# Optimization experiments

Measured on AMD Instinct MI355X. Metric: run time of the kernel, lower is better.

The kernel has to match this reference:

```python
import jax, jax.numpy as jnp
import numpy as np

N_NODES = 100000
N_EDGES = 1600000
D_IN = 128
D_OUT = 128


def setup_inputs() -> dict:
    key = jax.random.key(0)
    kx, ke, kw = jax.random.split(key, 3)
    x = jax.random.normal(kx, (N_NODES, D_IN), dtype=jnp.float32)
    edge_index = jax.random.randint(ke, (2, N_EDGES), 0, N_NODES, dtype=jnp.int32)
    W = jax.random.normal(kw, (D_IN, D_OUT), dtype=jnp.float32) / np.sqrt(D_IN)
    b = jnp.zeros((D_OUT,), dtype=jnp.float32)
    return {"x": x, "edge_index": edge_index, "W": W, "b": b}


def reference(x, edge_index, W, b):
    # PyG GCNConv: x' = D^{-1/2} (A + I) D^{-1/2} (x @ W) + b, then ReLU.
    n = x.shape[0]
    xw = x @ W  # linear transform first (as in GCNConv)
    # add self-loops
    loops = jnp.arange(n, dtype=edge_index.dtype)
    row = jnp.concatenate([edge_index[0], loops])  # source nodes
    col = jnp.concatenate([edge_index[1], loops])  # destination nodes
    # symmetric degree normalization (degree counted on destination, PyG-style)
    deg = jax.ops.segment_sum(jnp.ones_like(col, dtype=xw.dtype), col, num_segments=n)
    dinv = jnp.where(deg > 0, jax.lax.rsqrt(deg), 0.0)
    norm = dinv[row] * dinv[col]  # [E+N]
    # gather -> scale -> scatter-add
    msg = xw[row] * norm[:, None]  # [E+N, D_OUT]
    agg = jax.ops.segment_sum(msg, col, num_segments=n)  # [N, D_OUT]
    return jax.nn.relu(agg + b)
```

## Files before the change

### kernel.cpp

```cpp
#include <hip/hip_runtime.h>

#define DCH 128
#define T_PART 4096
#define B_MAX 512
#define CAPC 6144

typedef short bf16x8 __attribute__((ext_vector_type(8)));
typedef float f32x4 __attribute__((ext_vector_type(4)));

__device__ inline unsigned short f2bf(float f) {
    unsigned int u = __float_as_uint(f);
    unsigned int r = (u + 0x7fffu + ((u >> 16) & 1u)) >> 16;
    return (unsigned short)r;
}

__device__ inline void gload_lds16(const void* g, void* l) {
    __builtin_amdgcn_global_load_lds(
        (const __attribute__((address_space(1))) void*)g,
        (__attribute__((address_space(3))) void*)l, 16, 0, 0);
}

__global__ __launch_bounds__(512) void k_pg(const int* __restrict__ row,
                                            const int* __restrict__ col,
                                            unsigned int* __restrict__ coarse,
                                            int* __restrict__ gcount,
                                            const float* __restrict__ W,
                                            unsigned short* __restrict__ Wf,
                                            int E, int B, int nPart) {
    int tid = threadIdx.x;
    int wv = tid >> 6, lane = tid & 63;

    if (blockIdx.x >= nPart) {
        int frag = (blockIdx.x - nPart) * 8 + wv;
        if (frag < 32) {
            int nt = frag >> 2, ks = frag & 3;
            int nn = nt * 16 + (lane & 15);
            int k0 = ks * 32 + ((lane >> 4) * 8);
            unsigned short tmp[8];
#pragma unroll
            for (int j = 0; j < 8; ++j) tmp[j] = f2bf(W[(size_t)(k0 + j) * DCH + nn]);
            *(uint4*)&Wf[((size_t)frag * 64 + lane) * 8] = *(const uint4*)tmp;
        }
        return;
    }

    __shared__ unsigned int spack[T_PART];
    __shared__ unsigned short sbuck[T_PART];
    __shared__ int hist[B_MAX];
    __shared__ int basex[B_MAX];
    __shared__ int curx[B_MAX];
    __shared__ int wsum[8];
    int* gb = hist;

    int base_e = blockIdx.x * T_PART;
    int tileCnt = min(T_PART, E - base_e);

    hist[tid] = 0;
    __syncthreads();

    int er[8], ec[8];
#pragma unroll
    for (int i = 0; i < 8; ++i) {
        int e = base_e + tid + i * 512;
        if (e < E) {
            er[i] = row[e];
            ec[i] = col[e];
            atomicAdd(&hist[ec[i] >> 8], 1);
        } else {
            er[i] = -1;
            ec[i] = 0;
        }
    }
    __syncthreads();

    int v = hist[tid];
    int x2 = v;
#pragma unroll
    for (int o = 1; o < 64; o <<= 1) {
        int t = __shfl_up(x2, o, 64);
        if (lane >= o) x2 += t;
    }
    if (lane == 63) wsum[wv] = x2;
    __syncthreads();
    int add = 0;
    for (int w = 0; w < wv; ++w) add += wsum[w];
    int excl = x2 - v + add;
    basex[tid] = excl;
    curx[tid] = excl;
    gb[tid] = (tid < B && v > 0) ? atomicAdd(&gcount[tid], v) : 0;
    __syncthreads();

#pragma unroll
    for (int i = 0; i < 8; ++i) {
        if (er[i] >= 0) {
            int bb = ec[i] >> 8;
            int slot = atomicAdd(&curx[bb], 1);
            spack[slot] = ((unsigned int)er[i] << 8) | (unsigned int)(ec[i] & 255);
            sbuck[slot] = (unsigned short)bb;
        }
    }
    __syncthreads();

    for (int s = tid; s < tileCnt; s += 512) {
        int bb = sbuck[s];
        int dst = gb[bb] + (s - basex[bb]);
        if (dst < CAPC) coarse[(size_t)bb * CAPC + dst] = spack[s];
    }
}

__global__ __launch_bounds__(512) void k_cg(const unsigned int* __restrict__ coarse,
                                            const int* __restrict__ gcount,
                                            int* __restrict__ srow,
                                            int* __restrict__ off,
                                            float* __restrict__ dinvf,
                                            const float* __restrict__ x,
                                            const unsigned short* __restrict__ Wf,
                                            unsigned short* __restrict__ y,
                                            int n, int B) {
    __shared__ uint4 smem4[2048];
    char* smem = (char*)smem4;

    int tid = threadIdx.x;
    int wv = tid >> 6, lane = tid & 63;

    if (blockIdx.x < B) {
        unsigned int* ent = (unsigned int*)smem;
        int* h   = (int*)(smem + 24576);
        int* cur = (int*)(smem + 25600);
        int* red1 = (int*)(smem + 26624);
        int* red2 = (int*)(smem + 26656);
        int* bbase_p = (int*)(smem + 26672);

        int b = blockIdx.x;

        int part = 0;
        for (int i = tid; i < b; i += 512) part += gcount[i];
#pragma unroll
        for (int o = 1; o < 64; o <<= 1) part += __shfl_xor(part, o, 64);
        if (lane == 0) red1[wv] = part;
        if (tid < 256) h[tid] = 0;
        __syncthreads();
        if (tid == 0) {
            int s = 0;
            for (int w = 0; w < 8; ++w) s += red1[w];
            bbase_p[0] = s;
        }
        int cntb = min(gcount[b], CAPC);
        for (int s = tid; s < cntb; s += 512) ent[s] = coarse[(size_t)b * CAPC + s];
        __syncthreads();

        for (int s = tid; s < cntb; s += 512) atomicAdd(&h[ent[s] & 255], 1);
        __syncthreads();

        int x2 = 0, v = 0;
        if (tid < 256) {
            v = h[tid];
            x2 = v;
#pragma unroll
            for (int o = 1; o < 64; o <<= 1) {
                int t = __shfl_up(x2, o, 64);
                if (lane >= o) x2 += t;
            }
            if (lane == 63) red2[wv] = x2;
        }
        __syncthreads();
        int bbase = bbase_p[0];
        if (tid < 256) {
            int add = 0;
            for (int w = 0; w < wv; ++w) add += red2[w];
            int excl = x2 - v + add;
            cur[tid] = excl;
            int node = (b << 8) + tid;
            if (node < n) {
                off[node] = bbase + excl;
                dinvf[node] = rsqrtf((float)(v + 1));
            }
        }
        __syncthreads();

        for (int s = tid; s < cntb; s += 512) {
            unsigned int p = ent[s];
            int d = p & 255;
            int slot = atomicAdd(&cur[d], 1);
            srow[bbase + slot] = (int)(p >> 8);
        }
    } else {
        int blockRow = (blockIdx.x - B) * 64;

#pragma unroll
        for (int t = 0; t < 4; ++t) {
            int off2 = t * 8192 + wv * 1024 + lane * 16;
            int r = off2 >> 9;
            int gr = blockRow + r;
            if (gr >= n) gr = n - 1;
            int colb = (off2 & 511) ^ ((r & 7) << 4);
            const char* src = (const char*)x + (size_t)gr * 512 + colb;
            char* dst = smem + t * 8192 + wv * 1024;
            gload_lds16(src, dst);
        }
        __syncthreads();

        f32x4 acc[4];
        f32x4 zero = {0.f, 0.f, 0.f, 0.f};
#pragma unroll
        for (int t = 0; t < 4; ++t) acc[t] = zero;

        const bf16x8* wfv = (const bf16x8*)Wf;
        int rowL = (wv >> 1) * 16 + (lane & 15);
        int ntBase = (wv & 1) * 4;
        int q = lane >> 4;
        int swz = (rowL & 7) << 4;
#pragma unroll
        for (int ks = 0; ks < 4; ++ks) {
            int colb = ks * 128 + q * 32;
            float4 lo = *(const float4*)&smem[(rowL * 512 + colb) ^ swz];
            float4 hi = *(const float4*)&smem[(rowL * 512 + colb + 16) ^ swz];
            bf16x8 a;
            a[0] = (short)f2bf(lo.x); a[1] = (short)f2bf(lo.y);
            a[2] = (short)f2bf(lo.z); a[3] = (short)f2bf(lo.w);
            a[4] = (short)f2bf(hi.x); a[5] = (short)f2bf(hi.y);
            a[6] = (short)f2bf(hi.z); a[7] = (short)f2bf(hi.w);
#pragma unroll
            for (int nt2 = 0; nt2 < 4; ++nt2) {
                int nt = ntBase + nt2;
                bf16x8 bfr = wfv[(nt * 4 + ks) * 64 + lane];
                acc[nt2] = __builtin_amdgcn_mfma_f32_16x16x32_bf16(a, bfr, acc[nt2], 0, 0, 0);
            }
        }

        int rowBase = blockRow + (wv >> 1) * 16;
        int orow_base = rowBase + q * 4;
#pragma unroll
        for (int r = 0; r < 4; ++r) {
            int orow = orow_base + r;
            if (orow < n) {
#pragma unroll
                for (int nt2 = 0; nt2 < 4; ++nt2) {
                    int nt = ntBase + nt2;
                    y[(size_t)orow * DCH + nt * 16 + (lane & 15)] = f2bf(acc[nt2][r]);
                }
            }
        }
    }
}

__global__ __launch_bounds__(256) void k_agg(const uint4* __restrict__ y4,
                                             const int* __restrict__ srow,
                                             const int* __restrict__ off,
                                             const float* __restrict__ dinv,
                                             const float* __restrict__ b,
                                             float* __restrict__ out, int n, int E) {
    int i = blockIdx.x * 4 + (threadIdx.x >> 6);
    if (i >= n) return;
    int lane = threadIdx.x & 63;
    int q = lane >> 4;
    int l16 = lane & 15;
    int s = off[i];
    int e = (i + 1 < n) ? off[i + 1] : E;
    float di = dinv[i];

    float acc[8];
#pragma unroll
    for (int k = 0; k < 8; ++k) acc[k] = 0.f;

    if (q == 0) {
        uint4 v = y4[(size_t)i * 16 + l16];
        unsigned int p[4] = {v.x, v.y, v.z, v.w};
#pragma unroll
        for (int t = 0; t < 4; ++t) {
            acc[2 * t]     = fmaf(di, __uint_as_float(p[t] << 16), acc[2 * t]);
            acc[2 * t + 1] = fmaf(di, __uint_as_float(p[t] & 0xffff0000u), acc[2 * t + 1]);
        }
    }

    int j = s;
    for (; j + 16 <= e; j += 16) {
        int s0 = srow[j + q];
        int s1 = srow[j + 4 + q];
        int s2 = srow[j + 8 + q];
        int s3 = srow[j + 12 + q];
        float d0 = dinv[s0], d1 = dinv[s1], d2 = dinv[s2], d3 = dinv[s3];
        uint4 v0 = y4[(size_t)s0 * 16 + l16];
        uint4 v1 = y4[(size_t)s1 * 16 + l16];
        uint4 v2 = y4[(size_t)s2 * 16 + l16];
        uint4 v3 = y4[(size_t)s3 * 16 + l16];
        unsigned int p0[4] = {v0.x, v0.y, v0.z, v0.w};
        unsigned int p1[4] = {v1.x, v1.y, v1.z, v1.w};
        unsigned int p2[4] = {v2.x, v2.y, v2.z, v2.w};
        unsigned int p3[4] = {v3.x, v3.y, v3.z, v3.w};
#pragma unroll
        for (int t = 0; t < 4; ++t) {
            acc[2 * t]     = fmaf(d0, __uint_as_float(p0[t] << 16), acc[2 * t]);
            acc[2 * t + 1] = fmaf(d0, __uint_as_float(p0[t] & 0xffff0000u), acc[2 * t + 1]);
            acc[2 * t]     = fmaf(d1, __uint_as_float(p1[t] << 16), acc[2 * t]);
            acc[2 * t + 1] = fmaf(d1, __uint_as_float(p1[t] & 0xffff0000u), acc[2 * t + 1]);
            acc[2 * t]     = fmaf(d2, __uint_as_float(p2[t] << 16), acc[2 * t]);
            acc[2 * t + 1] = fmaf(d2, __uint_as_float(p2[t] & 0xffff0000u), acc[2 * t + 1]);
            acc[2 * t]     = fmaf(d3, __uint_as_float(p3[t] << 16), acc[2 * t]);
            acc[2 * t + 1] = fmaf(d3, __uint_as_float(p3[t] & 0xffff0000u), acc[2 * t + 1]);
        }
    }
    for (; j + 8 <= e; j += 8) {
        int s0 = srow[j + q];
        int s1 = srow[j + 4 + q];
        float d0 = dinv[s0], d1 = dinv[s1];
        uint4 v0 = y4[(size_t)s0 * 16 + l16];
        uint4 v1 = y4[(size_t)s1 * 16 + l16];
        unsigned int p0[4] = {v0.x, v0.y, v0.z, v0.w};
        unsigned int p1[4] = {v1.x, v1.y, v1.z, v1.w};
#pragma unroll
        for (int t = 0; t < 4; ++t) {
            acc[2 * t]     = fmaf(d0, __uint_as_float(p0[t] << 16), acc[2 * t]);
            acc[2 * t + 1] = fmaf(d0, __uint_as_float(p0[t] & 0xffff0000u), acc[2 * t + 1]);
            acc[2 * t]     = fmaf(d1, __uint_as_float(p1[t] << 16), acc[2 * t]);
            acc[2 * t + 1] = fmaf(d1, __uint_as_float(p1[t] & 0xffff0000u), acc[2 * t + 1]);
        }
    }
    for (; j + 4 <= e; j += 4) {
        int s0 = srow[j + q];
        float d0 = dinv[s0];
        uint4 v0 = y4[(size_t)s0 * 16 + l16];
        unsigned int p0[4] = {v0.x, v0.y, v0.z, v0.w};
#pragma unroll
        for (int t = 0; t < 4; ++t) {
            acc[2 * t]     = fmaf(d0, __uint_as_float(p0[t] << 16), acc[2 * t]);
            acc[2 * t + 1] = fmaf(d0, __uint_as_float(p0[t] & 0xffff0000u), acc[2 * t + 1]);
        }
    }
    if (j + q < e) {
        int s0 = srow[j + q];
        float d0 = dinv[s0];
        uint4 v0 = y4[(size_t)s0 * 16 + l16];
        unsigned int p0[4] = {v0.x, v0.y, v0.z, v0.w};
#pragma unroll
        for (int t = 0; t < 4; ++t) {
            acc[2 * t]     = fmaf(d0, __uint_as_float(p0[t] << 16), acc[2 * t]);
            acc[2 * t + 1] = fmaf(d0, __uint_as_float(p0[t] & 0xffff0000u), acc[2 * t + 1]);
        }
    }

#pragma unroll
    for (int k = 0; k < 8; ++k) {
        acc[k] += __shfl_xor(acc[k], 16, 64);
        acc[k] += __shfl_xor(acc[k], 32, 64);
    }

    if (q == 0) {
        float sc = di;
        int c0 = l16 * 8;
        float4 b0 = *(const float4*)&b[c0];
        float4 b1 = *(const float4*)&b[c0 + 4];
        f32x4 o0, o1;
        o0[0] = fmaxf(fmaf(sc, acc[0], b0.x), 0.f);
        o0[1] = fmaxf(fmaf(sc, acc[1], b0.y), 0.f);
        o0[2] = fmaxf(fmaf(sc, acc[2], b0.z), 0.f);
        o0[3] = fmaxf(fmaf(sc, acc[3], b0.w), 0.f);
        o1[0] = fmaxf(fmaf(sc, acc[4], b1.x), 0.f);
        o1[1] = fmaxf(fmaf(sc, acc[5], b1.y), 0.f);
        o1[2] = fmaxf(fmaf(sc, acc[6], b1.z), 0.f);
        o1[3] = fmaxf(fmaf(sc, acc[7], b1.w), 0.f);
        f32x4* orow = (f32x4*)&out[(size_t)i * DCH + c0];
        __builtin_nontemporal_store(o0, &orow[0]);
        __builtin_nontemporal_store(o1, &orow[1]);
    }
}

extern "C" void kernel_launch(void* const* d_in, const int* in_sizes, int n_in,
                              void* d_out, int out_size, void* d_ws, size_t ws_size,
                              hipStream_t stream) {
    const float* x = (const float*)d_in[0];
    const int* ei  = (const int*)d_in[1];
    const float* W = (const float*)d_in[2];
    const float* b = (const float*)d_in[3];
    float* out = (float*)d_out;

    int n = in_sizes[0] / DCH;
    int E = in_sizes[1] / 2;
    const int* row = ei;
    const int* col = ei + E;

    int B = (n + 255) / 256;

    char* ws = (char*)d_ws;
    size_t o = 0;
    auto alloc = [&](size_t bytes) -> void* {
        o = (o + 255) & ~(size_t)255;
        void* p = ws + o;
        o += bytes;
        return p;
    };
    float* dinvf = (float*)alloc((size_t)n * 4);
    int* off     = (int*)alloc((size_t)(n + 1) * 4);
    int* gcount  = (int*)alloc((size_t)B * 4);
    int* srow    = (int*)alloc((size_t)E * 4);
    unsigned int* coarse = (unsigned int*)alloc((size_t)B * CAPC * 4);
    unsigned short* Wf = (unsigned short*)alloc((size_t)DCH * DCH * 2);
    unsigned short* y  = (unsigned short*)alloc((size_t)n * DCH * 2);

    int nt = (E + T_PART - 1) / T_PART;
    int gemmBlocks = (n + 63) / 64;

    hipMemsetAsync(gcount, 0, (size_t)B * 4, stream);
    k_pg<<<nt + 4, 512, 0, stream>>>(row, col, coarse, gcount, W, Wf, E, B, nt);
    k_cg<<<B + gemmBlocks, 512, 0, stream>>>(coarse, gcount, srow, off, dinvf,
                                             x, Wf, y, n, B);
    k_agg<<<(n + 3) / 4, 256, 0, stream>>>((const uint4*)y, srow, off, dinvf,
                                           b, out, n, E);
}
```

Before: 201.4 us.

## Replace two-level bucket CSR build with global atomic histogram and scatter

Replaces the coarse bucket partition (local sort into fixed-capacity buckets, then per-bucket fine sort) with a direct CSR build: a per-node global atomic histogram, a per-block offset scan kernel, and a scatter kernel that claims slots with global atomics on per-node cursors. This removes the coarse intermediate buffer, its capacity limit, and the LDS sorting passes. In exchange it adds an extra kernel launch and two global atomics per edge, and the edge order within each node becomes nondeterministic.

```diff
diff --git a/kernel.cpp b/kernel.cpp
--- a/kernel.cpp
+++ b/kernel.cpp
@@ -1,9 +1,8 @@
 #include <hip/hip_runtime.h>
 
 #define DCH 128
-#define T_PART 4096
+#define T_EDGE 4096
 #define B_MAX 512
-#define CAPC 6144
 
 typedef short bf16x8 __attribute__((ext_vector_type(8)));
 typedef float f32x4 __attribute__((ext_vector_type(4)));
@@ -20,18 +19,17 @@
         (__attribute__((address_space(3))) void*)l, 16, 0, 0);
 }
 
-__global__ __launch_bounds__(512) void k_pg(const int* __restrict__ row,
-                                            const int* __restrict__ col,
-                                            unsigned int* __restrict__ coarse,
-                                            int* __restrict__ gcount,
-                                            const float* __restrict__ W,
-                                            unsigned short* __restrict__ Wf,
-                                            int E, int B, int nPart) {
+__global__ __launch_bounds__(512) void k_hist(const int* __restrict__ col,
+                                              int* __restrict__ cnt,
+                                              int* __restrict__ gcount,
+                                              const float* __restrict__ W,
+                                              unsigned short* __restrict__ Wf,
+                                              int E, int B, int nEB) {
     int tid = threadIdx.x;
     int wv = tid >> 6, lane = tid & 63;
 
-    if (blockIdx.x >= nPart) {
-        int frag = (blockIdx.x - nPart) * 8 + wv;
+    if (blockIdx.x >= nEB) {
+        int frag = (blockIdx.x - nEB) * 8 + wv;
         if (frag < 32) {
             int nt = frag >> 2, ks = frag & 3;
             int nn = nt * 16 + (lane & 15);
@@ -44,148 +42,109 @@
         return;
     }
 
-    __shared__ unsigned int spack[T_PART];
-    __shared__ unsigned short sbuck[T_PART];
-    __shared__ int hist[B_MAX];
-    __shared__ int basex[B_MAX];
-    __shared__ int curx[B_MAX];
-    __shared__ int wsum[8];
-    int* gb = hist;
-
-    int base_e = blockIdx.x * T_PART;
-    int tileCnt = min(T_PART, E - base_e);
-
-    hist[tid] = 0;
-    __syncthreads();
-
-    int er[8], ec[8];
+    __shared__ int bh[B_MAX];
+    bh[tid] = 0;
+    __syncthreads();
+
+    int base_e = blockIdx.x * T_EDGE;
 #pragma unroll
     for (int i = 0; i < 8; ++i) {
         int e = base_e + tid + i * 512;
         if (e < E) {
-            er[i] = row[e];
-            ec[i] = col[e];
-            atomicAdd(&hist[ec[i] >> 8], 1);
-        } else {
-            er[i] = -1;
-            ec[i] = 0;
-        }
-    }
-    __syncthreads();
-
-    int v = hist[tid];
-    int x2 = v;
-#pragma unroll
-    for (int o = 1; o < 64; o <<= 1) {
-        int t = __shfl_up(x2, o, 64);
-        if (lane >= o) x2 += t;
-    }
-    if (lane == 63) wsum[wv] = x2;
-    __syncthreads();
-    int add = 0;
-    for (int w = 0; w < wv; ++w) add += wsum[w];
-    int excl = x2 - v + add;
-    basex[tid] = excl;
-    curx[tid] = excl;
-    gb[tid] = (tid < B && v > 0) ? atomicAdd(&gcount[tid], v) : 0;
-    __syncthreads();
-
-#pragma unroll
-    for (int i = 0; i < 8; ++i) {
-        if (er[i] >= 0) {
-            int bb = ec[i] >> 8;
-            int slot = atomicAdd(&curx[bb], 1);
-            spack[slot] = ((unsigned int)er[i] << 8) | (unsigned int)(ec[i] & 255);
-            sbuck[slot] = (unsigned short)bb;
-        }
-    }
-    __syncthreads();
-
-    for (int s = tid; s < tileCnt; s += 512) {
-        int bb = sbuck[s];
-        int dst = gb[bb] + (s - basex[bb]);
-        if (dst < CAPC) coarse[(size_t)bb * CAPC + dst] = spack[s];
-    }
-}
-
-__global__ __launch_bounds__(512) void k_cg(const unsigned int* __restrict__ coarse,
-                                            const int* __restrict__ gcount,
-                                            int* __restrict__ srow,
-                                            int* __restrict__ off,
-                                            float* __restrict__ dinvf,
-                                            const float* __restrict__ x,
-                                            const unsigned short* __restrict__ Wf,
-                                            unsigned short* __restrict__ y,
-                                            int n, int B) {
+            int c = col[e];
+            atomicAdd(&cnt[c], 1);
+            atomicAdd(&bh[c >> 8], 1);
+        }
+    }
+    __syncthreads();
+    if (tid < B && bh[tid] > 0) atomicAdd(&gcount[tid], bh[tid]);
+}
+
+__global__ __launch_bounds__(512) void k_off(const int* __restrict__ cnt,
+                                             const int* __restrict__ gcount,
+                                             int* __restrict__ off,
+                                             int* __restrict__ cur,
+                                             float* __restrict__ dinvf,
+                                             int n, int B) {
+    __shared__ int red1[8], red2[4];
+    __shared__ int bbase_s;
+
+    int b = blockIdx.x;
+    int tid = threadIdx.x;
+    int wv = tid >> 6, lane = tid & 63;
+
+    int part = 0;
+    for (int i = tid; i < b; i += 512) part += gcount[i];
+#pragma unroll
+    for (int o = 1; o < 64; o <<= 1) part += __shfl_xor(part, o, 64);
+    if (lane == 0) red1[wv] = part;
+    __syncthreads();
+    if (tid == 0) {
+        int s = 0;
+        for (int w = 0; w < 8; ++w) s += red1[w];
+        bbase_s = s;
+    }
+    __syncthreads();
+
+    int x2 = 0, v = 0;
+    if (tid < 256) {
+        int node = (b << 8) + tid;
+        v = (node < n) ? cnt[node] : 0;
+        x2 = v;
+#pragma unroll
+        for (int o = 1; o < 64; o <<= 1) {
+            int t = __shfl_up(x2, o, 64);
+            if (lane >= o) x2 += t;
+        }
+        if (lane == 63) red2[wv] = x2;
+    }
+    __syncthreads();
+    if (tid < 256) {
+        int add = 0;
+        for (int w = 0; w < wv; ++w) add += red2[w];
+        int excl = x2 - v + add;
+        int node = (b << 8) + tid;
+        if (node < n) {
+            int o2 = bbase_s + excl;
+            off[node] = o2;
+            cur[node] = o2;
+            dinvf[node] = rsqrtf((float)(v + 1));
+        }
+    }
+}
+
+__global__ __launch_bounds__(512) void k_scat(const int* __restrict__ row,
+                                              const int* __restrict__ col,
+                                              int* __restrict__ cur,
+                                              int* __restrict__ srow,
+                                              const float* __restrict__ x,
+                                              const unsigned short* __restrict__ Wf,
+                                              unsigned short* __restrict__ y,
+                                              int E, int n, int nEB) {
     __shared__ uint4 smem4[2048];
     char* smem = (char*)smem4;
 
     int tid = threadIdx.x;
     int wv = tid >> 6, lane = tid & 63;
 
-    if (blockIdx.x < B) {
-        unsigned int* ent = (unsigned int*)smem;
-        int* h   = (int*)(smem + 24576);
-        int* cur = (int*)(smem + 25600);
-        int* red1 = (int*)(smem + 26624);
-        int* red2 = (int*)(smem + 26656);
-        int* bbase_p = (int*)(smem + 26672);
-
-        int b = blockIdx.x;
-
-        int part = 0;
-        for (int i = tid; i < b; i += 512) part += gcount[i];
-#pragma unroll
-        for (int o = 1; o < 64; o <<= 1) part += __shfl_xor(part, o, 64);
-        if (lane == 0) red1[wv] = part;
-        if (tid < 256) h[tid] = 0;
-        __syncthreads();
-        if (tid == 0) {
-            int s = 0;
-            for (int w = 0; w < 8; ++w) s += red1[w];
-            bbase_p[0] = s;
-        }
-        int cntb = min(gcount[b], CAPC);
-        for (int s = tid; s < cntb; s += 512) ent[s] = coarse[(size_t)b * CAPC + s];
-        __syncthreads();
-
-        for (int s = tid; s < cntb; s += 512) atomicAdd(&h[ent[s] & 255], 1);
-        __syncthreads();
-
-        int x2 = 0, v = 0;
-        if (tid < 256) {
-            v = h[tid];
-            x2 = v;
-#pragma unroll
-            for (int o = 1; o < 64; o <<= 1) {
-                int t = __shfl_up(x2, o, 64);
-                if (lane >= o) x2 += t;
-            }
-            if (lane == 63) red2[wv] = x2;
-        }
-        __syncthreads();
-        int bbase = bbase_p[0];
-        if (tid < 256) {
-            int add = 0;
-            for (int w = 0; w < wv; ++w) add += red2[w];
-            int excl = x2 - v + add;
-            cur[tid] = excl;
-            int node = (b << 8) + tid;
-            if (node < n) {
-                off[node] = bbase + excl;
-                dinvf[node] = rsqrtf((float)(v + 1));
-            }
-        }
-        __syncthreads();
-
-        for (int s = tid; s < cntb; s += 512) {
-            unsigned int p = ent[s];
-            int d = p & 255;
-            int slot = atomicAdd(&cur[d], 1);
-            srow[bbase + slot] = (int)(p >> 8);
-        }
+    if (blockIdx.x < nEB) {
+        int base_e = blockIdx.x * T_EDGE;
+        int er[8], ec[8];
+#pragma unroll
+        for (int i = 0; i < 8; ++i) {
+            int e = base_e + tid + i * 512;
+            er[i] = (e < E) ? row[e] : -1;
+            ec[i] = (e < E) ? col[e] : 0;
+        }
+        int sl[8];
+#pragma unroll
+        for (int i = 0; i < 8; ++i)
+            sl[i] = (er[i] >= 0) ? atomicAdd(&cur[ec[i]], 1) : 0;
+#pragma unroll
+        for (int i = 0; i < 8; ++i)
+            if (er[i] >= 0) srow[sl[i]] = er[i];
     } else {
-        int blockRow = (blockIdx.x - B) * 64;
+        int blockRow = (blockIdx.x - nEB) * 64;
 
 #pragma unroll
         for (int t = 0; t < 4; ++t) {
@@ -389,21 +348,23 @@
         o += bytes;
         return p;
     };
+    int* cnt     = (int*)alloc((size_t)(n + B) * 4);
+    int* gcount  = cnt + n;
     float* dinvf = (float*)alloc((size_t)n * 4);
     int* off     = (int*)alloc((size_t)(n + 1) * 4);
-    int* gcount  = (int*)alloc((size_t)B * 4);
+    int* cur     = (int*)alloc((size_t)n * 4);
     int* srow    = (int*)alloc((size_t)E * 4);
-    unsigned int* coarse = (unsigned int*)alloc((size_t)B * CAPC * 4);
     unsigned short* Wf = (unsigned short*)alloc((size_t)DCH * DCH * 2);
     unsigned short* y  = (unsigned short*)alloc((size_t)n * DCH * 2);
 
-    int nt = (E + T_PART - 1) / T_PART;
+    int nEB = (E + T_EDGE - 1) / T_EDGE;
     int gemmBlocks = (n + 63) / 64;
 
-    hipMemsetAsync(gcount, 0, (size_t)B * 4, stream);
-    k_pg<<<nt + 4, 512, 0, stream>>>(row, col, coarse, gcount, W, Wf, E, B, nt);
-    k_cg<<<B + gemmBlocks, 512, 0, stream>>>(coarse, gcount, srow, off, dinvf,
-                                             x, Wf, y, n, B);
+    hipMemsetAsync(cnt, 0, (size_t)(n + B) * 4, stream);
+    k_hist<<<nEB + 4, 512, 0, stream>>>(col, cnt, gcount, W, Wf, E, B, nEB);
+    k_off<<<B, 512, 0, stream>>>(cnt, gcount, off, cur, dinvf, n, B);
+    k_scat<<<nEB + gemmBlocks, 512, 0, stream>>>(row, col, cur, srow,
+                                                 x, Wf, y, E, n, nEB);
     k_agg<<<(n + 3) / 4, 256, 0, stream>>>((const uint4*)y, srow, off, dinvf,
                                            b, out, n, E);
 }
```

Result: slower. 331.9 us (+64.8%).

## Merge partition, GEMM and bucket-sort stages into one persistent cooperative kernel

Applied to the files above, without the earlier changes.

Replaces the separate partition and bucket-sort/GEMM launches with a single cooperative persistent kernel. Its blocks loop over edge-partition tiles and GEMM tiles, then meet at a grid-wide sync before the per-bucket fine sort. The memset and W conversion move into a small init kernel, and the partition tile size is halved so more tiles spread across the persistent grid. The aim is to cut launch gaps and overlap the GEMM with partitioning, at the cost of a grid barrier and limits on occupancy and grid size.

```diff
diff --git a/kernel.cpp b/kernel.cpp
--- a/kernel.cpp
+++ b/kernel.cpp
@@ -1,7 +1,10 @@
 #include <hip/hip_runtime.h>
+#include <hip/hip_cooperative_groups.h>
+
+namespace cg = cooperative_groups;
 
 #define DCH 128
-#define T_PART 4096
+#define T_PART 2048
 #define B_MAX 512
 #define CAPC 6144
 
@@ -20,110 +23,174 @@
         (__attribute__((address_space(3))) void*)l, 16, 0, 0);
 }
 
-__global__ __launch_bounds__(512) void k_pg(const int* __restrict__ row,
-                                            const int* __restrict__ col,
-                                            unsigned int* __restrict__ coarse,
-                                            int* __restrict__ gcount,
-                                            const float* __restrict__ W,
-                                            unsigned short* __restrict__ Wf,
-                                            int E, int B, int nPart) {
+__global__ __launch_bounds__(256) void k_init(const float* __restrict__ W,
+                                              unsigned short* __restrict__ Wf,
+                                              int* __restrict__ gcount, int B) {
+    int idx = blockIdx.x * 256 + threadIdx.x;
+    if (idx < B) gcount[idx] = 0;
+    int frag = blockIdx.x * 4 + (threadIdx.x >> 6);
+    if (frag < 32) {
+        int lane = threadIdx.x & 63;
+        int nt = frag >> 2, ks = frag & 3;
+        int nn = nt * 16 + (lane & 15);
+        int k0 = ks * 32 + ((lane >> 4) * 8);
+        unsigned short tmp[8];
+#pragma unroll
+        for (int j = 0; j < 8; ++j) tmp[j] = f2bf(W[(size_t)(k0 + j) * DCH + nn]);
+        *(uint4*)&Wf[((size_t)frag * 64 + lane) * 8] = *(const uint4*)tmp;
+    }
+}
+
+__global__ __launch_bounds__(512, 8) void k_pre(const int* __restrict__ row,
+                                                const int* __restrict__ col,
+                                                unsigned int* __restrict__ coarse,
+                                                int* __restrict__ gcount,
+                                                const float* __restrict__ x,
+                                                const unsigned short* __restrict__ Wf,
+                                                unsigned short* __restrict__ y,
+                                                int* __restrict__ srow,
+                                                int* __restrict__ off,
+                                                float* __restrict__ dinvf,
+                                                int E, int B, int nPart, int nGemm,
+                                                int n) {
+    __shared__ uint4 smem4[2048];
+    char* smem = (char*)smem4;
+
     int tid = threadIdx.x;
     int wv = tid >> 6, lane = tid & 63;
-
-    if (blockIdx.x >= nPart) {
-        int frag = (blockIdx.x - nPart) * 8 + wv;
-        if (frag < 32) {
-            int nt = frag >> 2, ks = frag & 3;
-            int nn = nt * 16 + (lane & 15);
-            int k0 = ks * 32 + ((lane >> 4) * 8);
-            unsigned short tmp[8];
-#pragma unroll
-            for (int j = 0; j < 8; ++j) tmp[j] = f2bf(W[(size_t)(k0 + j) * DCH + nn]);
-            *(uint4*)&Wf[((size_t)frag * 64 + lane) * 8] = *(const uint4*)tmp;
-        }
-        return;
-    }
-
-    __shared__ unsigned int spack[T_PART];
-    __shared__ unsigned short sbuck[T_PART];
-    __shared__ int hist[B_MAX];
-    __shared__ int basex[B_MAX];
-    __shared__ int curx[B_MAX];
-    __shared__ int wsum[8];
-    int* gb = hist;
-
-    int base_e = blockIdx.x * T_PART;
-    int tileCnt = min(T_PART, E - base_e);
-
-    hist[tid] = 0;
-    __syncthreads();
-
-    int er[8], ec[8];
-#pragma unroll
-    for (int i = 0; i < 8; ++i) {
-        int e = base_e + tid + i * 512;
-        if (e < E) {
-            er[i] = row[e];
-            ec[i] = col[e];
-            atomicAdd(&hist[ec[i] >> 8], 1);
+    cg::grid_group grid = cg::this_grid();
+    int G = gridDim.x;
+
+    for (int item = blockIdx.x; item < nPart + nGemm; item += G) {
+        __syncthreads();
+        if (item < nPart) {
+            unsigned int* spack   = (unsigned int*)smem;
+            unsigned short* sbuck = (unsigned short*)(smem + 8192);
+            int* hist  = (int*)(smem + 12288);
+            int* basex = (int*)(smem + 14336);
+            int* curx  = (int*)(smem + 16384);
+            int* wsum  = (int*)(smem + 18432);
+            int* gb = hist;
+
+            int base_e = item * T_PART;
+            int tileCnt = min(T_PART, E - base_e);
+
+            hist[tid] = 0;
+            __syncthreads();
+
+            int er[4], ec[4];
+#pragma unroll
+            for (int i = 0; i < 4; ++i) {
+                int e = base_e + tid + i * 512;
+                if (e < E) {
+                    er[i] = row[e];
+                    ec[i] = col[e];
+                    atomicAdd(&hist[ec[i] >> 8], 1);
+                } else {
+                    er[i] = -1;
+                    ec[i] = 0;
+                }
+            }
+            __syncthreads();
+
+            int v = hist[tid];
+            int x2 = v;
+#pragma unroll
+            for (int o = 1; o < 64; o <<= 1) {
+                int t = __shfl_up(x2, o, 64);
+                if (lane >= o) x2 += t;
+            }
+            if (lane == 63) wsum[wv] = x2;
+            __syncthreads();
+            int add = 0;
+            for (int w = 0; w < wv; ++w) add += wsum[w];
+            int excl = x2 - v + add;
+            basex[tid] = excl;
+            curx[tid] = excl;
+            gb[tid] = (tid < B && v > 0) ? atomicAdd(&gcount[tid], v) : 0;
+            __syncthreads();
+
+#pragma unroll
+            for (int i = 0; i < 4; ++i) {
+                if (er[i] >= 0) {
+                    int bb = ec[i] >> 8;
+                    int slot = atomicAdd(&curx[bb], 1);
+                    spack[slot] = ((unsigned int)er[i] << 8) | (unsigned int)(ec[i] & 255);
+                    sbuck[slot] = (unsigned short)bb;
+                }
+            }
+            __syncthreads();
+
+            for (int s = tid; s < tileCnt; s += 512) {
+                int bb = sbuck[s];
+                int dst = gb[bb] + (s - basex[bb]);
+                if (dst < CAPC) coarse[(size_t)bb * CAPC + dst] = spack[s];
+            }
         } else {
-            er[i] = -1;
-            ec[i] = 0;
-        }
-    }
-    __syncthreads();
-
-    int v = hist[tid];
-    int x2 = v;
-#pragma unroll
-    for (int o = 1; o < 64; o <<= 1) {
-        int t = __shfl_up(x2, o, 64);
-        if (lane >= o) x2 += t;
-    }
-    if (lane == 63) wsum[wv] = x2;
-    __syncthreads();
-    int add = 0;
-    for (int w = 0; w < wv; ++w) add += wsum[w];
-    int excl = x2 - v + add;
-    basex[tid] = excl;
-    curx[tid] = excl;
-    gb[tid] = (tid < B && v > 0) ? atomicAdd(&gcount[tid], v) : 0;
-    __syncthreads();
-
-#pragma unroll
-    for (int i = 0; i < 8; ++i) {
-        if (er[i] >= 0) {
-            int bb = ec[i] >> 8;
-            int slot = atomicAdd(&curx[bb], 1);
-            spack[slot] = ((unsigned int)er[i] << 8) | (unsigned int)(ec[i] & 255);
-            sbuck[slot] = (unsigned short)bb;
-        }
-    }
-    __syncthreads();
-
-    for (int s = tid; s < tileCnt; s += 512) {
-        int bb = sbuck[s];
-        int dst = gb[bb] + (s - basex[bb]);
-        if (dst < CAPC) coarse[(size_t)bb * CAPC + dst] = spack[s];
-    }
-}
-
-__global__ __launch_bounds__(512) void k_cg(const unsigned int* __restrict__ coarse,
-                                            const int* __restrict__ gcount,
-                                            int* __restrict__ srow,
-                                            int* __restrict__ off,
-                                            float* __restrict__ dinvf,
-                                            const float* __restrict__ x,
-                                            const unsigned short* __restrict__ Wf,
-                                            unsigned short* __restrict__ y,
-                                            int n, int B) {
-    __shared__ uint4 smem4[2048];
-    char* smem = (char*)smem4;
-
-    int tid = threadIdx.x;
-    int wv = tid >> 6, lane = tid & 63;
-
-    if (blockIdx.x < B) {
+            int blockRow = (item - nPart) * 64;
+
+#pragma unroll
+            for (int t = 0; t < 4; ++t) {
+                int off2 = t * 8192 + wv * 1024 + lane * 16;
+                int r = off2 >> 9;
+                int gr = blockRow + r;
+                if (gr >= n) gr = n - 1;
+                int colb = (off2 & 511) ^ ((r & 7) << 4);
+                const char* src = (const char*)x + (size_t)gr * 512 + colb;
+                char* dst = smem + t * 8192 + wv * 1024;
+                gload_lds16(src, dst);
+            }
+            __syncthreads();
+
+            f32x4 acc[4];
+            f32x4 zero = {0.f, 0.f, 0.f, 0.f};
+#pragma unroll
+            for (int t = 0; t < 4; ++t) acc[t] = zero;
+
+            const bf16x8* wfv = (const bf16x8*)Wf;
+            int rowL = (wv >> 1) * 16 + (lane & 15);
+            int ntBase = (wv & 1) * 4;
+            int q = lane >> 4;
+            int swz = (rowL & 7) << 4;
+#pragma unroll
+            for (int ks = 0; ks < 4; ++ks) {
+                int colb = ks * 128 + q * 32;
+                float4 lo = *(const float4*)&smem[(rowL * 512 + colb) ^ swz];
+                float4 hi = *(const float4*)&smem[(rowL * 512 + colb + 16) ^ swz];
+                bf16x8 a;
+                a[0] = (short)f2bf(lo.x); a[1] = (short)f2bf(lo.y);
+                a[2] = (short)f2bf(lo.z); a[3] = (short)f2bf(lo.w);
+                a[4] = (short)f2bf(hi.x); a[5] = (short)f2bf(hi.y);
+                a[6] = (short)f2bf(hi.z); a[7] = (short)f2bf(hi.w);
+#pragma unroll
+                for (int nt2 = 0; nt2 < 4; ++nt2) {
+                    int nt = ntBase + nt2;
+                    bf16x8 bfr = wfv[(nt * 4 + ks) * 64 + lane];
+                    acc[nt2] = __builtin_amdgcn_mfma_f32_16x16x32_bf16(a, bfr, acc[nt2], 0, 0, 0);
+                }
+            }
+
+            int rowBase = blockRow + (wv >> 1) * 16;
+            int orow_base = rowBase + q * 4;
+#pragma unroll
+            for (int r = 0; r < 4; ++r) {
+                int orow = orow_base + r;
+                if (orow < n) {
+#pragma unroll
+                    for (int nt2 = 0; nt2 < 4; ++nt2) {
+                        int nt = ntBase + nt2;
+                        y[(size_t)orow * DCH + nt * 16 + (lane & 15)] = f2bf(acc[nt2][r]);
+                    }
+                }
+            }
+        }
+    }
+
+    __threadfence();
+    grid.sync();
+
+    for (int item = blockIdx.x; item < B; item += G) {
+        __syncthreads();
         unsigned int* ent = (unsigned int*)smem;
         int* h   = (int*)(smem + 24576);
         int* cur = (int*)(smem + 25600);
@@ -131,7 +198,7 @@
         int* red2 = (int*)(smem + 26656);
         int* bbase_p = (int*)(smem + 26672);
 
-        int b = blockIdx.x;
+        int b = item;
 
         int part = 0;
         for (int i = tid; i < b; i += 512) part += gcount[i];
@@ -183,63 +250,6 @@
             int d = p & 255;
             int slot = atomicAdd(&cur[d], 1);
             srow[bbase + slot] = (int)(p >> 8);
-        }
-    } else {
-        int blockRow = (blockIdx.x - B) * 64;
-
-#pragma unroll
-        for (int t = 0; t < 4; ++t) {
-            int off2 = t * 8192 + wv * 1024 + lane * 16;
-            int r = off2 >> 9;
-            int gr = blockRow + r;
-            if (gr >= n) gr = n - 1;
-            int colb = (off2 & 511) ^ ((r & 7) << 4);
-            const char* src = (const char*)x + (size_t)gr * 512 + colb;
-            char* dst = smem + t * 8192 + wv * 1024;
-            gload_lds16(src, dst);
-        }
-        __syncthreads();
-
-        f32x4 acc[4];
-        f32x4 zero = {0.f, 0.f, 0.f, 0.f};
-#pragma unroll
-        for (int t = 0; t < 4; ++t) acc[t] = zero;
-
-        const bf16x8* wfv = (const bf16x8*)Wf;
-        int rowL = (wv >> 1) * 16 + (lane & 15);
-        int ntBase = (wv & 1) * 4;
-        int q = lane >> 4;
-        int swz = (rowL & 7) << 4;
-#pragma unroll
-        for (int ks = 0; ks < 4; ++ks) {
-            int colb = ks * 128 + q * 32;
-            float4 lo = *(const float4*)&smem[(rowL * 512 + colb) ^ swz];
-            float4 hi = *(const float4*)&smem[(rowL * 512 + colb + 16) ^ swz];
-            bf16x8 a;
-            a[0] = (short)f2bf(lo.x); a[1] = (short)f2bf(lo.y);
-            a[2] = (short)f2bf(lo.z); a[3] = (short)f2bf(lo.w);
-            a[4] = (short)f2bf(hi.x); a[5] = (short)f2bf(hi.y);
-            a[6] = (short)f2bf(hi.z); a[7] = (short)f2bf(hi.w);
-#pragma unroll
-            for (int nt2 = 0; nt2 < 4; ++nt2) {
-                int nt = ntBase + nt2;
-                bf16x8 bfr = wfv[(nt * 4 + ks) * 64 + lane];
-                acc[nt2] = __builtin_amdgcn_mfma_f32_16x16x32_bf16(a, bfr, acc[nt2], 0, 0, 0);
-            }
-        }
-
-        int rowBase = blockRow + (wv >> 1) * 16;
-        int orow_base = rowBase + q * 4;
-#pragma unroll
-        for (int r = 0; r < 4; ++r) {
-            int orow = orow_base + r;
-            if (orow < n) {
-#pragma unroll
-                for (int nt2 = 0; nt2 < 4; ++nt2) {
-                    int nt = ntBase + nt2;
-                    y[(size_t)orow * DCH + nt * 16 + (lane & 15)] = f2bf(acc[nt2][r]);
-                }
-            }
         }
     }
 }
@@ -397,13 +407,25 @@
     unsigned short* Wf = (unsigned short*)alloc((size_t)DCH * DCH * 2);
     unsigned short* y  = (unsigned short*)alloc((size_t)n * DCH * 2);
 
-    int nt = (E + T_PART - 1) / T_PART;
-    int gemmBlocks = (n + 63) / 64;
-
-    hipMemsetAsync(gcount, 0, (size_t)B * 4, stream);
-    k_pg<<<nt + 4, 512, 0, stream>>>(row, col, coarse, gcount, W, Wf, E, B, nt);
-    k_cg<<<B + gemmBlocks, 512, 0, stream>>>(coarse, gcount, srow, off, dinvf,
-                                             x, Wf, y, n, B);
+    int nPart = (E + T_PART - 1) / T_PART;
+    int nGemm = (n + 63) / 64;
+
+    int maxB = 0;
+    hipOccupancyMaxActiveBlocksPerMultiprocessor(&maxB, k_pre, 512, 0);
+    if (maxB < 1) maxB = 4;
+    long G = (long)maxB * 256;
+    if (G > 1024) G = 1024;
+    if (G > nPart + nGemm) G = nPart + nGemm;
+
+    k_init<<<8, 256, 0, stream>>>(W, Wf, gcount, B);
+
+    void* args[] = {(void*)&row, (void*)&col, (void*)&coarse, (void*)&gcount,
+                    (void*)&x, (void*)&Wf, (void*)&y, (void*)&srow, (void*)&off,
+                    (void*)&dinvf, (void*)&E, (void*)&B, (void*)&nPart,
+                    (void*)&nGemm, (void*)&n};
+    hipLaunchCooperativeKernel((void*)k_pre, dim3((unsigned)G), dim3(512),
+                               args, 0, stream);
+
     k_agg<<<(n + 3) / 4, 256, 0, stream>>>((const uint4*)y, srow, off, dinvf,
                                            b, out, n, E);
 }
```

After: 419.3 us. 108% more time.

## Split GEMM across partition and CSR kernels, move W convert into init kernel

Applied to the files above, without the earlier changes.

The hipMemsetAsync and the W-to-bf16 fragment conversion are replaced by a small init kernel. The x@W GEMM tiles are split in half: the first half now runs alongside the edge-partition blocks in k_pga and the second half alongside the bucket-CSR blocks in k_cg. This spreads the GEMM work so it overlaps both latency-bound sort stages rather than only one, and drops the separate memset launch. The cost is an extra kernel launch, and the partition kernel now uses a shared-memory union sized for the GEMM tile, which could change occupancy.

```diff
diff --git a/kernel.cpp b/kernel.cpp
--- a/kernel.cpp
+++ b/kernel.cpp
@@ -20,36 +20,108 @@
         (__attribute__((address_space(3))) void*)l, 16, 0, 0);
 }
 
-__global__ __launch_bounds__(512) void k_pg(const int* __restrict__ row,
-                                            const int* __restrict__ col,
-                                            unsigned int* __restrict__ coarse,
-                                            int* __restrict__ gcount,
-                                            const float* __restrict__ W,
-                                            unsigned short* __restrict__ Wf,
-                                            int E, int B, int nPart) {
+__global__ __launch_bounds__(256) void k_init(const float* __restrict__ W,
+                                              unsigned short* __restrict__ Wf,
+                                              int* __restrict__ gcount, int B) {
+    int idx = blockIdx.x * 256 + threadIdx.x;
+    if (idx < B) gcount[idx] = 0;
+    int frag = blockIdx.x * 4 + (threadIdx.x >> 6);
+    if (frag < 32) {
+        int lane = threadIdx.x & 63;
+        int nt = frag >> 2, ks = frag & 3;
+        int nn = nt * 16 + (lane & 15);
+        int k0 = ks * 32 + ((lane >> 4) * 8);
+        unsigned short tmp[8];
+#pragma unroll
+        for (int j = 0; j < 8; ++j) tmp[j] = f2bf(W[(size_t)(k0 + j) * DCH + nn]);
+        *(uint4*)&Wf[((size_t)frag * 64 + lane) * 8] = *(const uint4*)tmp;
+    }
+}
+
+__device__ inline void gemm_tile(char* smem, const float* __restrict__ x,
+                                 const unsigned short* __restrict__ Wf,
+                                 unsigned short* __restrict__ y,
+                                 int blockRow, int n, int wv, int lane) {
+#pragma unroll
+    for (int t = 0; t < 4; ++t) {
+        int off2 = t * 8192 + wv * 1024 + lane * 16;
+        int r = off2 >> 9;
+        int gr = blockRow + r;
+        if (gr >= n) gr = n - 1;
+        int colb = (off2 & 511) ^ ((r & 7) << 4);
+        const char* src = (const char*)x + (size_t)gr * 512 + colb;
+        char* dst = smem + t * 8192 + wv * 1024;
+        gload_lds16(src, dst);
+    }
+    __syncthreads();
+
+    f32x4 acc[4];
+    f32x4 zero = {0.f, 0.f, 0.f, 0.f};
+#pragma unroll
+    for (int t = 0; t < 4; ++t) acc[t] = zero;
+
+    const bf16x8* wfv = (const bf16x8*)Wf;
+    int rowL = (wv >> 1) * 16 + (lane & 15);
+    int ntBase = (wv & 1) * 4;
+    int q = lane >> 4;
+    int swz = (rowL & 7) << 4;
+#pragma unroll
+    for (int ks = 0; ks < 4; ++ks) {
+        int colb = ks * 128 + q * 32;
+        float4 lo = *(const float4*)&smem[(rowL * 512 + colb) ^ swz];
+        float4 hi = *(const float4*)&smem[(rowL * 512 + colb + 16) ^ swz];
+        bf16x8 a;
+        a[0] = (short)f2bf(lo.x); a[1] = (short)f2bf(lo.y);
+        a[2] = (short)f2bf(lo.z); a[3] = (short)f2bf(lo.w);
+        a[4] = (short)f2bf(hi.x); a[5] = (short)f2bf(hi.y);
+        a[6] = (short)f2bf(hi.z); a[7] = (short)f2bf(hi.w);
+#pragma unroll
+        for (int nt2 = 0; nt2 < 4; ++nt2) {
+            int nt = ntBase + nt2;
+            bf16x8 bfr = wfv[(nt * 4 + ks) * 64 + lane];
+            acc[nt2] = __builtin_amdgcn_mfma_f32_16x16x32_bf16(a, bfr, acc[nt2], 0, 0, 0);
+        }
+    }
+
+    int orow_base = blockRow + (wv >> 1) * 16 + q * 4;
+#pragma unroll
+    for (int r = 0; r < 4; ++r) {
+        int orow = orow_base + r;
+        if (orow < n) {
+#pragma unroll
+            for (int nt2 = 0; nt2 < 4; ++nt2) {
+                int nt = ntBase + nt2;
+                y[(size_t)orow * DCH + nt * 16 + (lane & 15)] = f2bf(acc[nt2][r]);
+            }
+        }
+    }
+}
+
+__global__ __launch_bounds__(512) void k_pga(const int* __restrict__ row,
+                                             const int* __restrict__ col,
+                                             unsigned int* __restrict__ coarse,
+                                             int* __restrict__ gcount,
+                                             const float* __restrict__ x,
+                                             const unsigned short* __restrict__ Wf,
+                                             unsigned short* __restrict__ y,
+                                             int E, int B, int nPart, int n) {
+    __shared__ uint4 smem4[2048];
+    char* smem = (char*)smem4;
+
     int tid = threadIdx.x;
     int wv = tid >> 6, lane = tid & 63;
 
     if (blockIdx.x >= nPart) {
-        int frag = (blockIdx.x - nPart) * 8 + wv;
-        if (frag < 32) {
-            int nt = frag >> 2, ks = frag & 3;
-            int nn = nt * 16 + (lane & 15);
-            int k0 = ks * 32 + ((lane >> 4) * 8);
-            unsigned short tmp[8];
-#pragma unroll
-            for (int j = 0; j < 8; ++j) tmp[j] = f2bf(W[(size_t)(k0 + j) * DCH + nn]);
-            *(uint4*)&Wf[((size_t)frag * 64 + lane) * 8] = *(const uint4*)tmp;
-        }
+        gemm_tile(smem, x, Wf, y, (blockIdx.x - nPart) * 64, n, wv, lane);
         return;
     }
 
-    __shared__ unsigned int spack[T_PART];
-    __shared__ unsigned short sbuck[T_PART];
-    __shared__ int hist[B_MAX];
-    __shared__ int basex[B_MAX];
-    __shared__ int curx[B_MAX];
-    __shared__ int wsum[8];
+    unsigned int* spack   = (unsigned int*)smem;
+    unsigned short* sbuck = (unsigned short*)(smem + 16384);
+    int* hist  = (int*)(smem + 24576);
+    int* basex = (int*)(smem + 26624);
+    int* curx  = (int*)(smem + 28672);
+    int* wsum  = (int*)(smem + 30720);
     int* gb = hist;
 
     int base_e = blockIdx.x * T_PART;
@@ -116,131 +188,77 @@
                                             const float* __restrict__ x,
                                             const unsigned short* __restrict__ Wf,
                                             unsigned short* __restrict__ y,
-                                            int n, int B) {
+                                            int n, int B, int gemmRow0) {
     __shared__ uint4 smem4[2048];
     char* smem = (char*)smem4;
 
     int tid = threadIdx.x;
     int wv = tid >> 6, lane = tid & 63;
 
-    if (blockIdx.x < B) {
-        unsigned int* ent = (unsigned int*)smem;
-        int* h   = (int*)(smem + 24576);
-        int* cur = (int*)(smem + 25600);
-        int* red1 = (int*)(smem + 26624);
-        int* red2 = (int*)(smem + 26656);
-        int* bbase_p = (int*)(smem + 26672);
-
-        int b = blockIdx.x;
-
-        int part = 0;
-        for (int i = tid; i < b; i += 512) part += gcount[i];
-#pragma unroll
-        for (int o = 1; o < 64; o <<= 1) part += __shfl_xor(part, o, 64);
-        if (lane == 0) red1[wv] = part;
-        if (tid < 256) h[tid] = 0;
-        __syncthreads();
-        if (tid == 0) {
-            int s = 0;
-            for (int w = 0; w < 8; ++w) s += red1[w];
-            bbase_p[0] = s;
-        }
-        int cntb = min(gcount[b], CAPC);
-        for (int s = tid; s < cntb; s += 512) ent[s] = coarse[(size_t)b * CAPC + s];
-        __syncthreads();
-
-        for (int s = tid; s < cntb; s += 512) atomicAdd(&h[ent[s] & 255], 1);
-        __syncthreads();
-
-        int x2 = 0, v = 0;
-        if (tid < 256) {
-            v = h[tid];
-            x2 = v;
-#pragma unroll
-            for (int o = 1; o < 64; o <<= 1) {
-                int t = __shfl_up(x2, o, 64);
-                if (lane >= o) x2 += t;
-            }
-            if (lane == 63) red2[wv] = x2;
-        }
-        __syncthreads();
-        int bbase = bbase_p[0];
-        if (tid < 256) {
-            int add = 0;
-            for (int w = 0; w < wv; ++w) add += red2[w];
-            int excl = x2 - v + add;
-            cur[tid] = excl;
-            int node = (b << 8) + tid;
-            if (node < n) {
-                off[node] = bbase + excl;
-                dinvf[node] = rsqrtf((float)(v + 1));
-            }
-        }
-        __syncthreads();
-
-        for (int s = tid; s < cntb; s += 512) {
-            unsigned int p = ent[s];
-            int d = p & 255;
-            int slot = atomicAdd(&cur[d], 1);
-            srow[bbase + slot] = (int)(p >> 8);
-        }
-    } else {
-        int blockRow = (blockIdx.x - B) * 64;
-
-#pragma unroll
-        for (int t = 0; t < 4; ++t) {
-            int off2 = t * 8192 + wv * 1024 + lane * 16;
-            int r = off2 >> 9;
-            int gr = blockRow + r;
-            if (gr >= n) gr = n - 1;
-            int colb = (off2 & 511) ^ ((r & 7) << 4);
-            const char* src = (const char*)x + (size_t)gr * 512 + colb;
-            char* dst = smem + t * 8192 + wv * 1024;
-            gload_lds16(src, dst);
-        }
-        __syncthreads();
-
-        f32x4 acc[4];
-        f32x4 zero = {0.f, 0.f, 0.f, 0.f};
-#pragma unroll
-        for (int t = 0; t < 4; ++t) acc[t] = zero;
-
-        const bf16x8* wfv = (const bf16x8*)Wf;
-        int rowL = (wv >> 1) * 16 + (lane & 15);
-        int ntBase = (wv & 1) * 4;
-        int q = lane >> 4;
-        int swz = (rowL & 7) << 4;
-#pragma unroll
-        for (int ks = 0; ks < 4; ++ks) {
-            int colb = ks * 128 + q * 32;
-            float4 lo = *(const float4*)&smem[(rowL * 512 + colb) ^ swz];
-            float4 hi = *(const float4*)&smem[(rowL * 512 + colb + 16) ^ swz];
-            bf16x8 a;
-            a[0] = (short)f2bf(lo.x); a[1] = (short)f2bf(lo.y);
-            a[2] = (short)f2bf(lo.z); a[3] = (short)f2bf(lo.w);
-            a[4] = (short)f2bf(hi.x); a[5] = (short)f2bf(hi.y);
-            a[6] = (short)f2bf(hi.z); a[7] = (short)f2bf(hi.w);
-#pragma unroll
-            for (int nt2 = 0; nt2 < 4; ++nt2) {
-                int nt = ntBase + nt2;
-                bf16x8 bfr = wfv[(nt * 4 + ks) * 64 + lane];
-                acc[nt2] = __builtin_amdgcn_mfma_f32_16x16x32_bf16(a, bfr, acc[nt2], 0, 0, 0);
-            }
-        }
-
-        int rowBase = blockRow + (wv >> 1) * 16;
-        int orow_base = rowBase + q * 4;
-#pragma unroll
-        for (int r = 0; r < 4; ++r) {
-            int orow = orow_base + r;
-            if (orow < n) {
-#pragma unroll
-                for (int nt2 = 0; nt2 < 4; ++nt2) {
-                    int nt = ntBase + nt2;
-                    y[(size_t)orow * DCH + nt * 16 + (lane & 15)] = f2bf(acc[nt2][r]);
-                }
-            }
-        }
+    if (blockIdx.x >= B) {
+        gemm_tile(smem, x, Wf, y, gemmRow0 + (blockIdx.x - B) * 64, n, wv, lane);
+        return;
+    }
+
+    unsigned int* ent = (unsigned int*)smem;
+    int* h   = (int*)(smem + 24576);
+    int* cur = (int*)(smem + 25600);
+    int* red1 = (int*)(smem + 26624);
+    int* red2 = (int*)(smem + 26656);
+    int* bbase_p = (int*)(smem + 26672);
+
+    int b = blockIdx.x;
+
+    int part = 0;
+    for (int i = tid; i < b; i += 512) part += gcount[i];
+#pragma unroll
+    for (int o = 1; o < 64; o <<= 1) part += __shfl_xor(part, o, 64);
+    if (lane == 0) red1[wv] = part;
+    if (tid < 256) h[tid] = 0;
+    __syncthreads();
+    if (tid == 0) {
+        int s = 0;
+        for (int w = 0; w < 8; ++w) s += red1[w];
+        bbase_p[0] = s;
+    }
+    int cntb = min(gcount[b], CAPC);
+    for (int s = tid; s < cntb; s += 512) ent[s] = coarse[(size_t)b * CAPC + s];
+    __syncthreads();
+
+    for (int s = tid; s < cntb; s += 512) atomicAdd(&h[ent[s] & 255], 1);
+    __syncthreads();
+
+    int x2 = 0, v = 0;
+    if (tid < 256) {
+        v = h[tid];
+        x2 = v;
+#pragma unroll
+        for (int o = 1; o < 64; o <<= 1) {
+            int t = __shfl_up(x2, o, 64);
+            if (lane >= o) x2 += t;
+        }
+        if (lane == 63) red2[wv] = x2;
+    }
+    __syncthreads();
+    int bbase = bbase_p[0];
+    if (tid < 256) {
+        int add = 0;
+        for (int w = 0; w < wv; ++w) add += red2[w];
+        int excl = x2 - v + add;
+        cur[tid] = excl;
+        int node = (b << 8) + tid;
+        if (node < n) {
+            off[node] = bbase + excl;
+            dinvf[node] = rsqrtf((float)(v + 1));
+        }
+    }
+    __syncthreads();
+
+    for (int s = tid; s < cntb; s += 512) {
+        unsigned int p = ent[s];
+        int d = p & 255;
+        int slot = atomicAdd(&cur[d], 1);
+        srow[bbase + slot] = (int)(p >> 8);
     }
 }
 
@@ -399,11 +417,15 @@
 
     int nt = (E + T_PART - 1) / T_PART;
     int gemmBlocks = (n + 63) / 64;
-
-    hipMemsetAsync(gcount, 0, (size_t)B * 4, stream);
-    k_pg<<<nt + 4, 512, 0, stream>>>(row, col, coarse, gcount, W, Wf, E, B, nt);
-    k_cg<<<B + gemmBlocks, 512, 0, stream>>>(coarse, gcount, srow, off, dinvf,
-                                             x, Wf, y, n, B);
+    int gA = gemmBlocks / 2;
+    int rowsA = gA * 64;
+    int gB = (n - rowsA + 63) / 64;
+
+    k_init<<<8, 256, 0, stream>>>(W, Wf, gcount, B);
+    k_pga<<<nt + gA, 512, 0, stream>>>(row, col, coarse, gcount,
+                                       x, Wf, y, E, B, nt, n);
+    k_cg<<<B + gB, 512, 0, stream>>>(coarse, gcount, srow, off, dinvf,
+                                     x, Wf, y, n, B, rowsA);
     k_agg<<<(n + 3) / 4, 256, 0, stream>>>((const uint4*)y, srow, off, dinvf,
                                            b, out, n, E);
 }
```

Result: no change. 201.2 us (-0.1%).
